# Kernel tuning notes

Hardware: AMD Instinct MI355X
Metric: run time of the kernel (lower is better)

The kernel has to match this reference:

```python
import jax, jax.numpy as jnp
import numpy as np


def _get_rel_pos(q_size, k_size, rel_pos):
    # table length is assumed == 2*max(q,k)-1 (no interpolation path)
    q_coords = jnp.arange(q_size)[:, None] * max(k_size / q_size, 1.0)
    k_coords = jnp.arange(k_size)[None, :] * max(q_size / k_size, 1.0)
    rel = (q_coords - k_coords + (k_size - 1) * max(q_size / k_size, 1.0)).astype(jnp.int32)
    return rel_pos[rel]  # (q_size, k_size, head_dim)


def setup_inputs() -> dict:
    key = jax.random.key(0)
    ks = jax.random.split(key, 7)
    B, N, C = 8, 1024, 768
    s = 0.02
    return {
        "x": jax.random.normal(ks[0], (B, N, C), jnp.float32),
        "qkv_w": jax.random.normal(ks[1], (3 * C, C), jnp.float32) * s,
        "qkv_b": jax.random.normal(ks[2], (3 * C,), jnp.float32) * s,
        "proj_w": jax.random.normal(ks[3], (C, C), jnp.float32) * s,
        "proj_b": jax.random.normal(ks[4], (C,), jnp.float32) * s,
        "rel_pos_h": jax.random.normal(ks[5], (63, 64), jnp.float32) * s,
        "rel_pos_w": jax.random.normal(ks[6], (63, 64), jnp.float32) * s,
        "H": 32,
        "W": 32,
    }


def reference(x, qkv_w, qkv_b, proj_w, proj_b, rel_pos_h, rel_pos_w, H, W):
    B, N, C = x.shape
    hd = rel_pos_h.shape[-1]
    nh = C // hd
    scale = hd ** -0.5

    qkv = (x @ qkv_w.T + qkv_b).reshape(B, N, 3, nh, hd)
    q, k, v = [qkv[:, :, i].transpose(0, 2, 1, 3) for i in range(3)]  # (B, nh, N, hd)

    # decomposed relative position bias on the last H*W query/key tokens (here all of them)
    Rh = _get_rel_pos(H, H, rel_pos_h)  # (H, H, hd)
    Rw = _get_rel_pos(W, W, rel_pos_w)  # (W, W, hd)
    r_q = q.reshape(B * nh, H, W, hd)
    rel_h = jnp.einsum("bhwc,hkc->bhwk", r_q, Rh)  # (B*nh, H, W, H)
    rel_w = jnp.einsum("bhwc,wkc->bhwk", r_q, Rw)  # (B*nh, H, W, W)
    bias = (rel_h[..., :, None] + rel_w[..., None, :]).reshape(B, nh, N, N)

    scores = jnp.einsum("bhqd,bhkd->bhqk", q * scale, k) + bias
    attn = jax.nn.softmax(scores, axis=-1)
    out = jnp.einsum("bhqk,bhkd->bhqd", attn, v)  # (B, nh, N, hd)
    out = out.transpose(0, 2, 1, 3).reshape(B, N, C)
    out = out @ proj_w.T + proj_b

    pre_kv = jnp.stack([k.reshape(B * nh, N, hd), v.reshape(B * nh, N, hd)])
    return out, pre_kv
```

## Files before the change

kernel.cpp:

```cpp
#include <hip/hip_runtime.h>
#include <hip/hip_bf16.h>
#include <stdint.h>

typedef __attribute__((ext_vector_type(8))) short bf16x8;
typedef __attribute__((ext_vector_type(4))) float f32x4;

#define LOG2E 1.4426950408889634f

__device__ __forceinline__ float exp2_fast(float x) {
  float r; asm("v_exp_f32 %0, %1" : "=v"(r) : "v"(x)); return r;
}

__device__ __forceinline__ float bf16bits_to_f32(short h) {
  union { uint32_t u; float f; } c;
  c.u = ((uint32_t)(unsigned short)h) << 16;
  return c.f;
}

__device__ __forceinline__ void gload_lds16(const void* g, void* l) {
  typedef __attribute__((address_space(1))) void gv_t;
  typedef __attribute__((address_space(3))) void lv_t;
  __builtin_amdgcn_global_load_lds((gv_t*)(uintptr_t)g,
                                   (lv_t*)(uint32_t)(uintptr_t)l, 16, 0, 0);
}

__global__ __launch_bounds__(256) void cvt_bf16(const float* __restrict__ src,
                                                __hip_bfloat16* __restrict__ dst, int n4) {
  int i = blockIdx.x * 256 + threadIdx.x;
  if (i < n4) {
    float4 f = ((const float4*)src)[i];
    union { ushort4 u; __hip_bfloat16 h[4]; } pk;
    pk.h[0] = __float2bfloat16(f.x);
    pk.h[1] = __float2bfloat16(f.y);
    pk.h[2] = __float2bfloat16(f.z);
    pk.h[3] = __float2bfloat16(f.w);
    ((ushort4*)dst)[i] = pk.u;
  }
}

__global__ __launch_bounds__(256) void cvt_bf16_pad(const float* __restrict__ src,
                                                    __hip_bfloat16* __restrict__ dst,
                                                    int n4src, int n4tot, float scale) {
  int i = blockIdx.x * 256 + threadIdx.x;
  if (i < n4tot) {
    float4 f = (i < n4src) ? ((const float4*)src)[i] : make_float4(0.f, 0.f, 0.f, 0.f);
    union { ushort4 u; __hip_bfloat16 h[4]; } pk;
    pk.h[0] = __float2bfloat16(f.x * scale);
    pk.h[1] = __float2bfloat16(f.y * scale);
    pk.h[2] = __float2bfloat16(f.z * scale);
    pk.h[3] = __float2bfloat16(f.w * scale);
    ((ushort4*)dst)[i] = pk.u;
  }
}

__global__ __launch_bounds__(256) void cvt_prekv(const __hip_bfloat16* __restrict__ xqkv,
                                                 float* __restrict__ prekv) {
  int gid = blockIdx.x * 256 + threadIdx.x;
  int o8 = gid * 8;
  int which = (o8 >= 6291456) ? 1 : 0;
  int r = o8 - which * 6291456;
  int bh = r >> 16;
  int t  = (r >> 6) & 1023;
  int d0 = r & 63;
  int b = bh / 12, h = bh - b * 12;
  const __hip_bfloat16* src = xqkv + (size_t)(b * 1024 + t) * 2304 +
                              (which ? 1536 : 768) + h * 64 + d0;
  bf16x8 v = *(const bf16x8*)src;
  float* dst = prekv + o8;
  float4 lo, hi;
  lo.x = bf16bits_to_f32(v[0]);
  lo.y = bf16bits_to_f32(v[1]);
  lo.z = bf16bits_to_f32(v[2]);
  lo.w = bf16bits_to_f32(v[3]);
  hi.x = bf16bits_to_f32(v[4]);
  hi.y = bf16bits_to_f32(v[5]);
  hi.z = bf16bits_to_f32(v[6]);
  hi.w = bf16bits_to_f32(v[7]);
  *(float4*)dst = lo;
  *(float4*)(dst + 4) = hi;
}

__device__ __forceinline__ void gemm_tile_compute(const __hip_bfloat16* __restrict__ A,
                                                  const __hip_bfloat16* __restrict__ Bm,
                                                  int K, int bm, int bn,
                                                  f32x4 acc[4][4], char* lbase) {
  const int tid = threadIdx.x;
  const int lane = tid & 63, w = tid >> 6;
  const int wr = w >> 1, wc = w & 1;
  const int rrow = lane & 15, g16 = lane >> 4;

  for (int k0 = 0; k0 < K; k0 += 32) {
    #pragma unroll
    for (int i = 0; i < 2; ++i) {
      int c = i * 4 + w;
      int b = c * 1024 + (lane << 4);
      int row = b >> 6;
      int cbs = ((b >> 4) & 3) ^ (row & 3);
      const char* ga = (const char*)(A + (size_t)(bm * 128 + row) * K + k0) + cbs * 16;
      gload_lds16(ga, lbase + c * 1024);
      const char* gb = (const char*)(Bm + (size_t)(bn * 128 + row) * K + k0) + cbs * 16;
      gload_lds16(gb, lbase + 8192 + c * 1024);
    }
    asm volatile("s_waitcnt vmcnt(0)" ::: "memory");
    __syncthreads();

    bf16x8 af[4], bfr[4];
    #pragma unroll
    for (int i = 0; i < 4; ++i) {
      int row = wr * 64 + i * 16 + rrow;
      af[i] = *(const bf16x8*)(lbase + row * 64 + ((g16 * 16) ^ ((row & 3) << 4)));
      int col = wc * 64 + i * 16 + rrow;
      bfr[i] = *(const bf16x8*)(lbase + 8192 + col * 64 + ((g16 * 16) ^ ((col & 3) << 4)));
    }
    __builtin_amdgcn_s_setprio(1);
    #pragma unroll
    for (int i = 0; i < 4; ++i)
      #pragma unroll
      for (int j = 0; j < 4; ++j)
        acc[i][j] = __builtin_amdgcn_mfma_f32_16x16x32_bf16(af[i], bfr[j], acc[i][j], 0, 0, 0);
    __builtin_amdgcn_s_setprio(0);
    __syncthreads();
  }
}

__global__ __launch_bounds__(256) void gemm_qkv_kernel(
    const __hip_bfloat16* __restrict__ xb, const __hip_bfloat16* __restrict__ wqkv,
    const float* __restrict__ qkv_b, __hip_bfloat16* __restrict__ xqkv) {
  __shared__ char smem[16384];
  f32x4 acc[4][4];
  const f32x4 z4 = {0.f, 0.f, 0.f, 0.f};
  #pragma unroll
  for (int i = 0; i < 4; ++i)
    #pragma unroll
    for (int j = 0; j < 4; ++j) acc[i][j] = z4;

  const int bn = blockIdx.x, bm = blockIdx.y;
  gemm_tile_compute(xb, wqkv, 768, bm, bn, acc, smem);

  const int lane = threadIdx.x & 63, w = threadIdx.x >> 6;
  const int wr = w >> 1, wc = w & 1;
  const int col0 = lane & 15, g = lane >> 4;
  #pragma unroll
  for (int j = 0; j < 4; ++j) {
    int n = bn * 128 + wc * 64 + j * 16 + col0;
    float bias = qkv_b[n];
    #pragma unroll
    for (int i = 0; i < 4; ++i) {
      #pragma unroll
      for (int r = 0; r < 4; ++r) {
        int m = bm * 128 + wr * 64 + i * 16 + g * 4 + r;
        xqkv[(size_t)m * 2304 + n] = __float2bfloat16(acc[i][j][r] + bias);
      }
    }
  }
}

__global__ __launch_bounds__(256) void gemm_proj_kernel(
    const __hip_bfloat16* __restrict__ Ows, const __hip_bfloat16* __restrict__ wproj,
    const float* __restrict__ proj_b, float* __restrict__ out) {
  __shared__ char smem[16384];
  f32x4 acc[4][4];
  const f32x4 z4 = {0.f, 0.f, 0.f, 0.f};
  #pragma unroll
  for (int i = 0; i < 4; ++i)
    #pragma unroll
    for (int j = 0; j < 4; ++j) acc[i][j] = z4;

  const int bn = blockIdx.x, bm = blockIdx.y;
  gemm_tile_compute(Ows, wproj, 768, bm, bn, acc, smem);

  const int lane = threadIdx.x & 63, w = threadIdx.x >> 6;
  const int wr = w >> 1, wc = w & 1;
  const int col0 = lane & 15, g = lane >> 4;
  #pragma unroll
  for (int j = 0; j < 4; ++j) {
    int n = bn * 128 + wc * 64 + j * 16 + col0;
    float bias = proj_b[n];
    #pragma unroll
    for (int i = 0; i < 4; ++i) {
      #pragma unroll
      for (int r = 0; r < 4; ++r) {
        int m = bm * 128 + wr * 64 + i * 16 + g * 4 + r;
        out[(size_t)m * 768 + n] = acc[i][j][r] + bias;
      }
    }
  }
}

#define VSWZ(hd) ((((hd) ^ ((hd) >> 3)) & 7) << 4)
__global__ __launch_bounds__(256, 3) void flash_attn(
    const __hip_bfloat16* __restrict__ xqkv, const __hip_bfloat16* __restrict__ rphb,
    const __hip_bfloat16* __restrict__ rpwb, __hip_bfloat16* __restrict__ Ows) {
  __shared__ alignas(16) char smem[49152];
  float* s_relh = (float*)smem;
  char*  s_kt   = smem + 16384;
  char*  s_vt   = smem + 24576;
  char*  s_pt   = smem + 32768;
  float* s_rw   = (float*)(smem + 32768);

  const int tid = threadIdx.x, lane = tid & 63, w = tid >> 6;
  const int g16 = lane >> 4, c16 = lane & 15;
  const int bid = blockIdx.x;
  const int qt = bid / 96, bh = bid - qt * 96;
  const int q0 = qt * 128;
  const int b = bh / 12, head = bh - b * 12;
  const __hip_bfloat16* Qb = xqkv + (size_t)b * 1024 * 2304 + head * 64;
  const __hip_bfloat16* Kb = Qb + 768;
  const __hip_bfloat16* Vb = Qb + 1536;

  bf16x8 qf[2][2];
  {
    const __hip_bfloat16* qp = Qb + (size_t)(q0 + w * 32 + c16) * 2304 + g16 * 8;
    qf[0][0] = *(const bf16x8*)qp;
    qf[0][1] = *(const bf16x8*)(qp + 32);
    qf[1][0] = *(const bf16x8*)(qp + 16 * 2304);
    qf[1][1] = *(const bf16x8*)(qp + 16 * 2304 + 32);
  }

  const f32x4 z4 = {0.f, 0.f, 0.f, 0.f};

  {
    f32x4 gh[2][4], gw[2][4];
    #pragma unroll
    for (int mb = 0; mb < 2; ++mb)
      #pragma unroll
      for (int nf = 0; nf < 4; ++nf) { gh[mb][nf] = z4; gw[mb][nf] = z4; }
    #pragma unroll
    for (int kc = 0; kc < 2; ++kc) {
      #pragma unroll
      for (int nf = 0; nf < 4; ++nf) {
        int j = nf * 16 + c16;
        bf16x8 th = *(const bf16x8*)(rphb + j * 64 + kc * 32 + g16 * 8);
        bf16x8 tw = *(const bf16x8*)(rpwb + j * 64 + kc * 32 + g16 * 8);
        gh[0][nf] = __builtin_amdgcn_mfma_f32_16x16x32_bf16(qf[0][kc], th, gh[0][nf], 0, 0, 0);
        gh[1][nf] = __builtin_amdgcn_mfma_f32_16x16x32_bf16(qf[1][kc], th, gh[1][nf], 0, 0, 0);
        gw[0][nf] = __builtin_amdgcn_mfma_f32_16x16x32_bf16(qf[0][kc], tw, gw[0][nf], 0, 0, 0);
        gw[1][nf] = __builtin_amdgcn_mfma_f32_16x16x32_bf16(qf[1][kc], tw, gw[1][nf], 0, 0, 0);
      }
    }
    const int hq = (q0 >> 5) + w;
    #pragma unroll
    for (int mb = 0; mb < 2; ++mb) {
      #pragma unroll
      for (int nf = 0; nf < 4; ++nf) {
        int j = nf * 16 + c16;
        int khh = hq - j + 31;
        #pragma unroll
        for (int r = 0; r < 4; ++r) {
          int rowin = mb * 16 + g16 * 4 + r;
          int lrow = w * 32 + rowin;
          if (khh >= 0 && khh < 32) s_relh[lrow * 32 + khh] = gh[mb][nf][r];
          int kww = rowin - j + 31;
          if (kww >= 0 && kww < 32) s_rw[lrow * 32 + kww] = gw[mb][nf][r];
        }
      }
    }
  }
  asm volatile("s_waitcnt lgkmcnt(0)" ::: "memory");
  float rw0[2][4], rw1[2][4];
  #pragma unroll
  for (int rb = 0; rb < 2; ++rb)
    #pragma unroll
    for (int r = 0; r < 4; ++r) {
      int lrow = w * 32 + rb * 16 + g16 * 4 + r;
      rw0[rb][r] = s_rw[lrow * 32 + c16];
      rw1[rb][r] = s_rw[lrow * 32 + 16 + c16];
    }

  f32x4 o[2][4];
  float m_r[2][4], l_r[2][4];
  #pragma unroll
  for (int rb = 0; rb < 2; ++rb) {
    #pragma unroll
    for (int hf = 0; hf < 4; ++hf) o[rb][hf] = z4;
    #pragma unroll
    for (int r = 0; r < 4; ++r) { m_r[rb][r] = -1e30f; l_r[rb][r] = 0.f; }
  }

  const float SCALE2 = 0.125f * LOG2E;
  const int kp = tid >> 3;
  const int hd0 = (tid & 7) * 8;

  for (int kt0 = 0; kt0 < 1024; kt0 += 64) {
    #pragma unroll
    for (int i = 0; i < 2; ++i) {
      int c = w * 2 + i;
      int row = c * 8 + (lane >> 3);
      int cbs = (lane & 7) ^ (row & 7);
      const char* g = (const char*)(Kb + (size_t)(kt0 + row) * 2304) + cbs * 16;
      gload_lds16(g, s_kt + c * 1024);
    }
    asm volatile("" ::: "memory");
    const __hip_bfloat16* vr = Vb + (size_t)(kt0 + 2 * kp) * 2304 + hd0;
    bf16x8 va = *(const bf16x8*)vr;
    bf16x8 vb = *(const bf16x8*)(vr + 2304);
    asm volatile("s_waitcnt vmcnt(2)" ::: "memory");
    __builtin_amdgcn_s_barrier();

    f32x4 s[2][4];
    #pragma unroll
    for (int rb = 0; rb < 2; ++rb)
      #pragma unroll
      for (int kf = 0; kf < 4; ++kf) s[rb][kf] = z4;
    __builtin_amdgcn_s_setprio(1);
    #pragma unroll
    for (int kc = 0; kc < 2; ++kc) {
      #pragma unroll
      for (int kf = 0; kf < 4; ++kf) {
        int key = kf * 16 + c16;
        int byte = key * 128 + (((kc * 32 + g16 * 8) * 2) ^ ((key & 7) << 4));
        bf16x8 kfr = *(const bf16x8*)(s_kt + byte);
        s[0][kf] = __builtin_amdgcn_mfma_f32_16x16x32_bf16(qf[0][kc], kfr, s[0][kf], 0, 0, 0);
        s[1][kf] = __builtin_amdgcn_mfma_f32_16x16x32_bf16(qf[1][kc], kfr, s[1][kf], 0, 0, 0);
      }
    }
    __builtin_amdgcn_s_setprio(0);

    asm volatile("s_waitcnt vmcnt(0)" ::: "memory");
    #pragma unroll
    for (int j = 0; j < 8; ++j) {
      int hd = hd0 + j;
      union { ushort2 u2; uint32_t u; } pk;
      pk.u2.x = (unsigned short)va[j];
      pk.u2.y = (unsigned short)vb[j];
      *(uint32_t*)(s_vt + hd * 128 + ((4 * kp) ^ VSWZ(hd))) = pk.u;
    }

    int kh0 = kt0 >> 5;
    f32x4 facv[2];
    #pragma unroll
    for (int rb = 0; rb < 2; ++rb) {
      float rh0[4], rh1[4];
      #pragma unroll
      for (int r = 0; r < 4; ++r) {
        int lrow = w * 32 + rb * 16 + g16 * 4 + r;
        float2 rh = *(const float2*)&s_relh[lrow * 32 + kh0];
        rh0[r] = rh.x; rh1[r] = rh.y;
      }
      #pragma unroll
      for (int kf = 0; kf < 4; ++kf)
        #pragma unroll
        for (int r = 0; r < 4; ++r)
          s[rb][kf][r] = fmaf(s[rb][kf][r], SCALE2,
                              ((kf >> 1) ? rh1[r] : rh0[r]) +
                              ((kf & 1) ? rw1[rb][r] : rw0[rb][r]));
      #pragma unroll
      for (int r = 0; r < 4; ++r) {
        float tm = fmaxf(fmaxf(s[rb][0][r], s[rb][1][r]), fmaxf(s[rb][2][r], s[rb][3][r]));
        tm = fmaxf(tm, __shfl_xor(tm, 1));
        tm = fmaxf(tm, __shfl_xor(tm, 2));
        tm = fmaxf(tm, __shfl_xor(tm, 4));
        tm = fmaxf(tm, __shfl_xor(tm, 8));
        float mold = m_r[rb][r];
        float mnew = fmaxf(mold, tm);
        float fac = exp2_fast(mold - mnew);
        m_r[rb][r] = mnew;
        facv[rb][r] = fac;
        float psum = 0.f;
        #pragma unroll
        for (int kf = 0; kf < 4; ++kf) {
          float p = exp2_fast(s[rb][kf][r] - mnew);
          s[rb][kf][r] = p;
          psum += p;
        }
        psum += __shfl_xor(psum, 1);
        psum += __shfl_xor(psum, 2);
        psum += __shfl_xor(psum, 4);
        psum += __shfl_xor(psum, 8);
        l_r[rb][r] = fmaf(l_r[rb][r], fac, psum);
      }
    }
    bool nr = (facv[0][0] == 1.f) & (facv[0][1] == 1.f) & (facv[0][2] == 1.f) &
              (facv[0][3] == 1.f) & (facv[1][0] == 1.f) & (facv[1][1] == 1.f) &
              (facv[1][2] == 1.f) & (facv[1][3] == 1.f);
    if (!__all(nr)) {
      #pragma unroll
      for (int rb = 0; rb < 2; ++rb)
        #pragma unroll
        for (int hf = 0; hf < 4; ++hf) o[rb][hf] *= facv[rb];
    }

    #pragma unroll
    for (int rb = 0; rb < 2; ++rb)
      #pragma unroll
      for (int kf = 0; kf < 4; ++kf) {
        int key = kf * 16 + c16;
        #pragma unroll
        for (int r = 0; r < 4; ++r) {
          int prow = rb * 16 + g16 * 4 + r;
          int byte = w * 4096 + prow * 128 + ((key * 2) ^ ((prow & 7) << 4));
          *(__hip_bfloat16*)(s_pt + byte) = __float2bfloat16(s[rb][kf][r]);
        }
      }

    asm volatile("s_waitcnt lgkmcnt(0)" ::: "memory");
    __builtin_amdgcn_s_barrier();

    __builtin_amdgcn_s_setprio(1);
    #pragma unroll
    for (int kc = 0; kc < 2; ++kc) {
      bf16x8 pf[2];
      #pragma unroll
      for (int rb = 0; rb < 2; ++rb) {
        int prow = rb * 16 + c16;
        int byte = w * 4096 + prow * 128 + (((kc * 32 + g16 * 8) * 2) ^ ((prow & 7) << 4));
        pf[rb] = *(const bf16x8*)(s_pt + byte);
      }
      #pragma unroll
      for (int hf = 0; hf < 4; ++hf) {
        int hd = hf * 16 + c16;
        int byte = hd * 128 + (((kc * 32 + g16 * 8) * 2) ^ VSWZ(hd));
        bf16x8 vf = *(const bf16x8*)(s_vt + byte);
        o[0][hf] = __builtin_amdgcn_mfma_f32_16x16x32_bf16(pf[0], vf, o[0][hf], 0, 0, 0);
        o[1][hf] = __builtin_amdgcn_mfma_f32_16x16x32_bf16(pf[1], vf, o[1][hf], 0, 0, 0);
      }
    }
    __builtin_amdgcn_s_setprio(0);
  }

  #pragma unroll
  for (int rb = 0; rb < 2; ++rb) {
    #pragma unroll
    for (int r = 0; r < 4; ++r) {
      int row = q0 + w * 32 + rb * 16 + g16 * 4 + r;
      float inv = 1.0f / l_r[rb][r];
      size_t base = ((size_t)b * 1024 + row) * 768 + head * 64;
      #pragma unroll
      for (int hf = 0; hf < 4; ++hf)
        Ows[base + hf * 16 + c16] = __float2bfloat16(o[rb][hf][r] * inv);
    }
  }
}

extern "C" void kernel_launch(void* const* d_in, const int* in_sizes, int n_in,
                              void* d_out, int out_size, void* d_ws, size_t ws_size,
                              hipStream_t stream) {
  const float* x      = (const float*)d_in[0];
  const float* qkv_w  = (const float*)d_in[1];
  const float* qkv_b  = (const float*)d_in[2];
  const float* proj_w = (const float*)d_in[3];
  const float* proj_b = (const float*)d_in[4];
  const float* rph    = (const float*)d_in[5];
  const float* rpw    = (const float*)d_in[6];

  char* ws = (char*)d_ws;
  __hip_bfloat16* xb    = (__hip_bfloat16*)(ws);
  __hip_bfloat16* wqkv  = (__hip_bfloat16*)(ws + 12582912);
  __hip_bfloat16* wproj = (__hip_bfloat16*)(ws + 16121856);
  __hip_bfloat16* xqkv  = (__hip_bfloat16*)(ws + 17301504);
  __hip_bfloat16* rphb  = (__hip_bfloat16*)(ws + 55050240);
  __hip_bfloat16* rpwb  = (__hip_bfloat16*)(ws + 55058432);
  __hip_bfloat16* Ows   = xb;

  float* out   = (float*)d_out;
  float* prekv = out + 6291456;

  cvt_bf16<<<6144, 256, 0, stream>>>(x, xb, 1572864);
  cvt_bf16<<<1728, 256, 0, stream>>>(qkv_w, wqkv, 442368);
  cvt_bf16<<<576, 256, 0, stream>>>(proj_w, wproj, 147456);
  cvt_bf16_pad<<<4, 256, 0, stream>>>(rph, rphb, 1008, 1024, LOG2E);
  cvt_bf16_pad<<<4, 256, 0, stream>>>(rpw, rpwb, 1008, 1024, LOG2E);
  gemm_qkv_kernel<<<dim3(18, 64), 256, 0, stream>>>(xb, wqkv, qkv_b, xqkv);
  cvt_prekv<<<6144, 256, 0, stream>>>(xqkv, prekv);
  flash_attn<<<768, 256, 0, stream>>>(xqkv, rphb, rpwb, Ows);
  gemm_proj_kernel<<<dim3(6, 64), 256, 0, stream>>>(Ows, wproj, proj_b, out);
}
```

Baseline: 370.8 us.

## Fuse pre_kv fp32 write into QKV GEMM epilogue and use head-major Q/K/V layout

The QKV GEMM epilogue now scatters results directly into head-major Q, K and V bf16 buffers and writes the fp32 pre_kv output itself. This removes the separate cvt_prekv kernel and its extra pass over the K/V data. Flash attention now reads contiguous 64-element rows per head instead of rows strided by 2304. The epilogue stores become scattered 2-byte and 4-byte writes, which may coalesce poorly, and pre_kv now keeps full fp32 values where it previously held bf16-rounded ones.

```diff
diff --git a/kernel.cpp b/kernel.cpp
--- a/kernel.cpp
+++ b/kernel.cpp
@@ -9,12 +9,6 @@
 
 __device__ __forceinline__ float exp2_fast(float x) {
   float r; asm("v_exp_f32 %0, %1" : "=v"(r) : "v"(x)); return r;
-}
-
-__device__ __forceinline__ float bf16bits_to_f32(short h) {
-  union { uint32_t u; float f; } c;
-  c.u = ((uint32_t)(unsigned short)h) << 16;
-  return c.f;
 }
 
 __device__ __forceinline__ void gload_lds16(const void* g, void* l) {
@@ -53,33 +47,6 @@
   }
 }
 
-__global__ __launch_bounds__(256) void cvt_prekv(const __hip_bfloat16* __restrict__ xqkv,
-                                                 float* __restrict__ prekv) {
-  int gid = blockIdx.x * 256 + threadIdx.x;
-  int o8 = gid * 8;
-  int which = (o8 >= 6291456) ? 1 : 0;
-  int r = o8 - which * 6291456;
-  int bh = r >> 16;
-  int t  = (r >> 6) & 1023;
-  int d0 = r & 63;
-  int b = bh / 12, h = bh - b * 12;
-  const __hip_bfloat16* src = xqkv + (size_t)(b * 1024 + t) * 2304 +
-                              (which ? 1536 : 768) + h * 64 + d0;
-  bf16x8 v = *(const bf16x8*)src;
-  float* dst = prekv + o8;
-  float4 lo, hi;
-  lo.x = bf16bits_to_f32(v[0]);
-  lo.y = bf16bits_to_f32(v[1]);
-  lo.z = bf16bits_to_f32(v[2]);
-  lo.w = bf16bits_to_f32(v[3]);
-  hi.x = bf16bits_to_f32(v[4]);
-  hi.y = bf16bits_to_f32(v[5]);
-  hi.z = bf16bits_to_f32(v[6]);
-  hi.w = bf16bits_to_f32(v[7]);
-  *(float4*)dst = lo;
-  *(float4*)(dst + 4) = hi;
-}
-
 __device__ __forceinline__ void gemm_tile_compute(const __hip_bfloat16* __restrict__ A,
                                                   const __hip_bfloat16* __restrict__ Bm,
                                                   int K, int bm, int bn,
@@ -125,7 +92,9 @@
 
 __global__ __launch_bounds__(256) void gemm_qkv_kernel(
     const __hip_bfloat16* __restrict__ xb, const __hip_bfloat16* __restrict__ wqkv,
-    const float* __restrict__ qkv_b, __hip_bfloat16* __restrict__ xqkv) {
+    const float* __restrict__ qkv_b,
+    __hip_bfloat16* __restrict__ Qws, __hip_bfloat16* __restrict__ Kws,
+    __hip_bfloat16* __restrict__ Vws, float* __restrict__ prekv) {
   __shared__ char smem[16384];
   f32x4 acc[4][4];
   const f32x4 z4 = {0.f, 0.f, 0.f, 0.f};
@@ -144,12 +113,25 @@
   for (int j = 0; j < 4; ++j) {
     int n = bn * 128 + wc * 64 + j * 16 + col0;
     float bias = qkv_b[n];
+    int which = n / 768;
+    int head = (n >> 6) % 12;
+    int d = n & 63;
     #pragma unroll
     for (int i = 0; i < 4; ++i) {
       #pragma unroll
       for (int r = 0; r < 4; ++r) {
         int m = bm * 128 + wr * 64 + i * 16 + g * 4 + r;
-        xqkv[(size_t)m * 2304 + n] = __float2bfloat16(acc[i][j][r] + bias);
+        float v = acc[i][j][r] + bias;
+        int b = m >> 10, t = m & 1023;
+        size_t idx = ((size_t)(b * 12 + head) << 16) + (t << 6) + d;
+        __hip_bfloat16 hv = __float2bfloat16(v);
+        if (which == 0) {
+          Qws[idx] = hv;
+        } else if (which == 1) {
+          Kws[idx] = hv; prekv[idx] = v;
+        } else {
+          Vws[idx] = hv; prekv[6291456 + idx] = v;
+        }
       }
     }
   }
@@ -189,7 +171,8 @@
 
 #define VSWZ(hd) ((((hd) ^ ((hd) >> 3)) & 7) << 4)
 __global__ __launch_bounds__(256, 3) void flash_attn(
-    const __hip_bfloat16* __restrict__ xqkv, const __hip_bfloat16* __restrict__ rphb,
+    const __hip_bfloat16* __restrict__ Qws, const __hip_bfloat16* __restrict__ Kws,
+    const __hip_bfloat16* __restrict__ Vws, const __hip_bfloat16* __restrict__ rphb,
     const __hip_bfloat16* __restrict__ rpwb, __hip_bfloat16* __restrict__ Ows) {
   __shared__ alignas(16) char smem[49152];
   float* s_relh = (float*)smem;
@@ -204,17 +187,15 @@
   const int qt = bid / 96, bh = bid - qt * 96;
   const int q0 = qt * 128;
   const int b = bh / 12, head = bh - b * 12;
-  const __hip_bfloat16* Qb = xqkv + (size_t)b * 1024 * 2304 + head * 64;
-  const __hip_bfloat16* Kb = Qb + 768;
-  const __hip_bfloat16* Vb = Qb + 1536;
+  const size_t bhbase = (size_t)bh << 16;
 
   bf16x8 qf[2][2];
   {
-    const __hip_bfloat16* qp = Qb + (size_t)(q0 + w * 32 + c16) * 2304 + g16 * 8;
+    const __hip_bfloat16* qp = Qws + bhbase + (size_t)(q0 + w * 32 + c16) * 64 + g16 * 8;
     qf[0][0] = *(const bf16x8*)qp;
     qf[0][1] = *(const bf16x8*)(qp + 32);
-    qf[1][0] = *(const bf16x8*)(qp + 16 * 2304);
-    qf[1][1] = *(const bf16x8*)(qp + 16 * 2304 + 32);
+    qf[1][0] = *(const bf16x8*)(qp + 16 * 64);
+    qf[1][1] = *(const bf16x8*)(qp + 16 * 64 + 32);
   }
 
   const f32x4 z4 = {0.f, 0.f, 0.f, 0.f};
@@ -287,13 +268,13 @@
       int c = w * 2 + i;
       int row = c * 8 + (lane >> 3);
       int cbs = (lane & 7) ^ (row & 7);
-      const char* g = (const char*)(Kb + (size_t)(kt0 + row) * 2304) + cbs * 16;
+      const char* g = (const char*)(Kws + bhbase + (size_t)(kt0 + row) * 64) + cbs * 16;
       gload_lds16(g, s_kt + c * 1024);
     }
     asm volatile("" ::: "memory");
-    const __hip_bfloat16* vr = Vb + (size_t)(kt0 + 2 * kp) * 2304 + hd0;
+    const __hip_bfloat16* vr = Vws + bhbase + (size_t)(kt0 + 2 * kp) * 64 + hd0;
     bf16x8 va = *(const bf16x8*)vr;
-    bf16x8 vb = *(const bf16x8*)(vr + 2304);
+    bf16x8 vb = *(const bf16x8*)(vr + 64);
     asm volatile("s_waitcnt vmcnt(2)" ::: "memory");
     __builtin_amdgcn_s_barrier();
 
@@ -447,7 +428,9 @@
   __hip_bfloat16* xb    = (__hip_bfloat16*)(ws);
   __hip_bfloat16* wqkv  = (__hip_bfloat16*)(ws + 12582912);
   __hip_bfloat16* wproj = (__hip_bfloat16*)(ws + 16121856);
-  __hip_bfloat16* xqkv  = (__hip_bfloat16*)(ws + 17301504);
+  __hip_bfloat16* Qws   = (__hip_bfloat16*)(ws + 17301504);
+  __hip_bfloat16* Kws   = (__hip_bfloat16*)(ws + 29884416);
+  __hip_bfloat16* Vws   = (__hip_bfloat16*)(ws + 42467328);
   __hip_bfloat16* rphb  = (__hip_bfloat16*)(ws + 55050240);
   __hip_bfloat16* rpwb  = (__hip_bfloat16*)(ws + 55058432);
   __hip_bfloat16* Ows   = xb;
@@ -460,8 +443,7 @@
   cvt_bf16<<<576, 256, 0, stream>>>(proj_w, wproj, 147456);
   cvt_bf16_pad<<<4, 256, 0, stream>>>(rph, rphb, 1008, 1024, LOG2E);
   cvt_bf16_pad<<<4, 256, 0, stream>>>(rpw, rpwb, 1008, 1024, LOG2E);
-  gemm_qkv_kernel<<<dim3(18, 64), 256, 0, stream>>>(xb, wqkv, qkv_b, xqkv);
-  cvt_prekv<<<6144, 256, 0, stream>>>(xqkv, prekv);
-  flash_attn<<<768, 256, 0, stream>>>(xqkv, rphb, rpwb, Ows);
+  gemm_qkv_kernel<<<dim3(18, 64), 256, 0, stream>>>(xb, wqkv, qkv_b, Qws, Kws, Vws, prekv);
+  flash_attn<<<768, 256, 0, stream>>>(Qws, Kws, Vws, rphb, rpwb, Ows);
   gemm_proj_kernel<<<dim3(6, 64), 256, 0, stream>>>(Ows, wproj, proj_b, out);
 }
```

New measurement: 367.2 us. No clear change (-1.0%).
